# Kernel tuning notes

Measured on AMD Instinct MI355X. Metric: run time of the kernel, lower is better.

The kernel has to match this reference:

```python
import jax, jax.numpy as jnp
import numpy as np

N_PATHOLOGY = 14      # NUM_PATHOLOGY_NODES (CheXpert/NIH pathology count)
NEG_SLOPE = 0.2       # PyG GATv2Conv default negative_slope


def gatv2_layer(x, src, dst, n_nodes, Wl, bl, Wr, br, att, bias, concat):
    """PyG GATv2Conv (share_weights=False, dropout inactive in eval).
    Wl/bl: source (lin_l) transform; Wr/br: target (lin_r) transform.
    att: [H, C] attention vector; bias: output bias.
    """
    H, C = att.shape
    xl = (x @ Wl + bl).reshape(-1, H, C)   # [N, H, C] source features
    xr = (x @ Wr + br).reshape(-1, H, C)   # [N, H, C] target features
    xj = xl[src]                            # [E, H, C] gathered source msgs
    xi = xr[dst]                            # [E, H, C] gathered targets
    s = jax.nn.leaky_relu(xi + xj, NEG_SLOPE)
    e = jnp.einsum('ehc,hc->eh', s, att)    # [E, H] raw attention logits
    # segment softmax over incoming edges of each destination node
    m = jax.ops.segment_max(e, dst, num_segments=n_nodes)      # [N, H]
    e = jnp.exp(e - m[dst])
    denom = jax.ops.segment_sum(e, dst, num_segments=n_nodes)  # [N, H]
    alpha = e / (denom[dst] + 1e-16)
    out = jax.ops.segment_sum(alpha[:, :, None] * xj, dst, num_segments=n_nodes)
    out = out.reshape(n_nodes, H * C) if concat else out.mean(axis=1)
    return out + bias


def setup_inputs() -> dict:
    key = jax.random.key(0)
    ks = jax.random.split(key, 16)
    N, E, D, H = 10000, 50000, 768, 4
    s = 0.02
    inp = {
        'x': jax.random.normal(ks[0], (N, D), jnp.float32),
        'edge_index': jax.random.randint(ks[1], (2, E), 0, N, jnp.int32),
        # layer 1: in=768 -> heads=4, out=768 (concat -> 3072)
        'Wl1': jax.random.normal(ks[2], (D, H * D), jnp.float32) * s,
        'bl1': jnp.zeros((H * D,), jnp.float32),
        'Wr1': jax.random.normal(ks[3], (D, H * D), jnp.float32) * s,
        'br1': jnp.zeros((H * D,), jnp.float32),
        'att1': jax.random.normal(ks[4], (H, D), jnp.float32) * s,
        'bias1': jnp.zeros((H * D,), jnp.float32),
        # layer 2: in=3072 -> heads=1, out=768 (mean/no-concat)
        'Wl2': jax.random.normal(ks[5], (H * D, D), jnp.float32) * s,
        'bl2': jnp.zeros((D,), jnp.float32),
        'Wr2': jax.random.normal(ks[6], (H * D, D), jnp.float32) * s,
        'br2': jnp.zeros((D,), jnp.float32),
        'att2': jax.random.normal(ks[7], (1, D), jnp.float32) * s,
        'bias2': jnp.zeros((D,), jnp.float32),
    }
    return inp


def reference(x, edge_index, Wl1, bl1, Wr1, br1, att1, bias1,
              Wl2, bl2, Wr2, br2, att2, bias2):
    n = x.shape[0]
    # PyG GATv2Conv adds self loops by default
    loops = jnp.arange(n, dtype=edge_index.dtype)
    src = jnp.concatenate([edge_index[0], loops])
    dst = jnp.concatenate([edge_index[1], loops])
    h = gatv2_layer(x, src, dst, n, Wl1, bl1, Wr1, br1, att1, bias1, True)
    h = jax.nn.relu(h)  # dropout is identity in eval mode
    out = gatv2_layer(h, src, dst, n, Wl2, bl2, Wr2, br2, att2, bias2, False)
    return out[:N_PATHOLOGY]
```

## Files before the change

### kernel.cpp

```cpp
#include <hip/hip_runtime.h>
#include <cstdint>
#include <cstddef>

#define N_PATH 14
#define NEG_SLOPE 0.2f
#define BINW 128

using u16 = unsigned short;
using u32 = unsigned int;
typedef __attribute__((ext_vector_type(4))) float f32x4;
typedef __attribute__((ext_vector_type(8))) short bf16x8;

__device__ __forceinline__ float lrelu(float v) { return v > 0.f ? v : NEG_SLOPE * v; }
__device__ __forceinline__ u16 f2bf(float f) {
    union { float f; u32 u; } c; c.f = f;
    return (u16)((c.u + 0x7FFFu + ((c.u >> 16) & 1u)) >> 16);
}
__device__ __forceinline__ float bf2f(u16 v) {
    union { u32 u; float f; } c; c.u = ((u32)v) << 16; return c.f;
}

__global__ void k_init(int* __restrict__ mapBC, int nMap,
                       u32* __restrict__ z, int nZ)
{
    int stride = gridDim.x * blockDim.x;
    int i0 = blockIdx.x * blockDim.x + threadIdx.x;
    for (int i = i0; i < nMap; i += stride) mapBC[i] = -1;
    for (int i = i0; i < nZ; i += stride) z[i] = 0;
}

__global__ void k_build2(const int* __restrict__ esrc, const int* __restrict__ edst,
                         int E, int Nn,
                         int* __restrict__ mapB, int* __restrict__ listB,
                         int* __restrict__ cnt,
                         int* __restrict__ deg2, int* __restrict__ e2bin,
                         int capB)
{
    int e = blockIdx.x * blockDim.x + threadIdx.x;
    int ET = E + Nn;
    if (e >= ET) return;
    int s, d;
    if (e < E) { s = esrc[e]; d = edst[e]; } else { s = e - E; d = s; }
    if (d >= N_PATH) return;
    int slot = atomicAdd(&deg2[d], 1);
    if (slot < BINW) e2bin[d * BINW + slot] = s;
    int old = atomicCAS(&mapB[s], -1, -2);
    if (old == -1) {
        int idx = atomicAdd(&cnt[0], 1);
        if (idx < capB) listB[idx] = s;
        mapB[s] = idx;
    }
}

__global__ void k_build1(const int* __restrict__ esrc, const int* __restrict__ edst,
                         int E, int Nn,
                         const int* __restrict__ mapB,
                         int* __restrict__ mapC, int* __restrict__ listC,
                         int* __restrict__ cnt,
                         int* __restrict__ deg1, int* __restrict__ e1bin,
                         int capB, int capC)
{
    int e = blockIdx.x * blockDim.x + threadIdx.x;
    int ET = E + Nn;
    if (e >= ET) return;
    int s, d;
    if (e < E) { s = esrc[e]; d = edst[e]; } else { s = e - E; d = s; }
    int b = mapB[d];
    if (b < 0 || b >= capB) return;
    int slot = atomicAdd(&deg1[b], 1);
    if (slot < BINW) e1bin[b * BINW + slot] = s;
    int old = atomicCAS(&mapC[s], -1, -2);
    if (old == -1) {
        int idx = atomicAdd(&cnt[1], 1);
        if (idx < capC) listC[idx] = s;
        mapC[s] = idx;
    }
}

__device__ __forceinline__
void gemm_tile(const void* __restrict__ A, int lda, int aF32,
               const int* __restrict__ gather,
               const float* __restrict__ W, int ldw, int nColOff,
               const float* __restrict__ bias,
               void* __restrict__ Cout, int ldc, int mode, bool addBias,
               const int* __restrict__ cnt, int cntIdx, int capM,
               int bx, int by, int k0, int kchunk,
               u16* __restrict__ As, u16* __restrict__ Bs)
{
    int M = cnt[cntIdx]; if (M > capM) M = capM;
    int m0 = by * 64;
    if (m0 >= M) return;
    int n0 = bx * 64;
    int t = threadIdx.x;
    int lane = t & 63, wave = t >> 6;
    int wr = wave >> 1, wc = wave & 1;
    int lrow = lane & 15, lhi = lane >> 4;

    int chunk = t & 7;
    int rowp[2], aRow[2], wIdx[2];
    #pragma unroll
    for (int p = 0; p < 2; ++p) {
        rowp[p] = p * 32 + (t >> 3);
        int ar = m0 + rowp[p]; if (ar >= M) ar = M - 1;
        aRow[p] = gather ? gather[ar] : ar;
        wIdx[p] = rowp[p] * 64 + ((chunk ^ (rowp[p] & 7)) << 3);
    }
    int bk = t >> 4;
    int bn = (t & 15) << 2;

    int aIdx[2][2], bIdx[2][2];
    #pragma unroll
    for (int mi = 0; mi < 2; ++mi)
        #pragma unroll
        for (int ks = 0; ks < 2; ++ks) {
            int ra = wr * 32 + mi * 16 + lrow;
            aIdx[mi][ks] = ra * 64 + ((((ks << 2) | lhi) ^ (ra & 7)) << 3);
            int rb = wc * 32 + mi * 16 + lrow;
            bIdx[mi][ks] = rb * 64 + ((((ks << 2) | lhi) ^ (rb & 7)) << 3);
        }

    f32x4 acc[2][2];
    #pragma unroll
    for (int i = 0; i < 2; ++i)
        #pragma unroll
        for (int j = 0; j < 2; ++j)
            acc[i][j] = (f32x4){0.f, 0.f, 0.f, 0.f};

    for (int kt = 0; kt < kchunk; kt += 64) {
        int kb = k0 + kt;
        #pragma unroll
        for (int p = 0; p < 2; ++p) {
            uint4 av;
            if (aF32) {
                const float* ap = (const float*)A + (size_t)aRow[p] * lda + kb + chunk * 8;
                float4 f0 = *reinterpret_cast<const float4*>(ap);
                float4 f1 = *reinterpret_cast<const float4*>(ap + 4);
                av.x = (u32)f2bf(f0.x) | ((u32)f2bf(f0.y) << 16);
                av.y = (u32)f2bf(f0.z) | ((u32)f2bf(f0.w) << 16);
                av.z = (u32)f2bf(f1.x) | ((u32)f2bf(f1.y) << 16);
                av.w = (u32)f2bf(f1.z) | ((u32)f2bf(f1.w) << 16);
            } else {
                av = *reinterpret_cast<const uint4*>((const u16*)A + (size_t)aRow[p] * lda + kb + chunk * 8);
            }
            *reinterpret_cast<uint4*>(&As[wIdx[p]]) = av;
        }
        #pragma unroll
        for (int p = 0; p < 4; ++p) {
            int kk = p * 16 + bk;
            const float* wp = W + (size_t)(kb + kk) * ldw + nColOff + n0 + bn;
            float4 wv = *reinterpret_cast<const float4*>(wp);
            float wa[4] = {wv.x, wv.y, wv.z, wv.w};
            #pragma unroll
            for (int j = 0; j < 4; ++j) {
                int n = bn + j;
                int pc = (kk & 7) | ((((kk >> 3) & 7) ^ (n & 7)) << 3);
                Bs[n * 64 + pc] = f2bf(wa[j]);
            }
        }
        __syncthreads();
        #pragma unroll
        for (int ks = 0; ks < 2; ++ks) {
            bf16x8 a0 = *reinterpret_cast<const bf16x8*>(&As[aIdx[0][ks]]);
            bf16x8 a1 = *reinterpret_cast<const bf16x8*>(&As[aIdx[1][ks]]);
            bf16x8 b0 = *reinterpret_cast<const bf16x8*>(&Bs[bIdx[0][ks]]);
            bf16x8 b1 = *reinterpret_cast<const bf16x8*>(&Bs[bIdx[1][ks]]);
            acc[0][0] = __builtin_amdgcn_mfma_f32_16x16x32_bf16(a0, b0, acc[0][0], 0, 0, 0);
            acc[0][1] = __builtin_amdgcn_mfma_f32_16x16x32_bf16(a0, b1, acc[0][1], 0, 0, 0);
            acc[1][0] = __builtin_amdgcn_mfma_f32_16x16x32_bf16(a1, b0, acc[1][0], 0, 0, 0);
            acc[1][1] = __builtin_amdgcn_mfma_f32_16x16x32_bf16(a1, b1, acc[1][1], 0, 0, 0);
        }
        __syncthreads();
    }

    #pragma unroll
    for (int mi = 0; mi < 2; ++mi)
        #pragma unroll
        for (int ni = 0; ni < 2; ++ni) {
            int gc = n0 + wc * 32 + ni * 16 + lrow;
            float bv = addBias ? bias[gc] : 0.f;
            #pragma unroll
            for (int j = 0; j < 4; ++j) {
                int gr = m0 + wr * 32 + mi * 16 + lhi * 4 + j;
                if (gr < M) {
                    float v = acc[mi][ni][j] + bv;
                    if (mode == 2) ((u16*)Cout)[(size_t)gr * ldc + gc] = f2bf(v);
                    else           atomicAdd(&((float*)Cout)[(size_t)gr * ldc + gc], v);
                }
            }
        }
}

__global__ __launch_bounds__(256)
void k_gemm1(const float* __restrict__ x,
             const int* __restrict__ listC, const int* __restrict__ listB,
             const float* __restrict__ Wl1, const float* __restrict__ Wr1,
             const float* __restrict__ bl1, const float* __restrict__ br1,
             u16* __restrict__ XL1, u16* __restrict__ XR1,
             const int* __restrict__ cnt, int capC, int capB)
{
    __shared__ __align__(16) u16 As[64 * 64];
    __shared__ __align__(16) u16 Bs[64 * 64];
    int partA = 48 * (capC / 64);
    int bid = blockIdx.x;
    if (bid < partA) {
        gemm_tile(x, 768, 1, listC, Wl1, 3072, 0, bl1, XL1, 3072, 2, true,
                  cnt, 1, capC, bid % 48, bid / 48, 0, 768, As, Bs);
    } else {
        bid -= partA;
        gemm_tile(x, 768, 1, listB, Wr1, 3072, 0, br1, XR1, 3072, 2, true,
                  cnt, 0, capB, bid % 48, bid / 48, 0, 768, As, Bs);
    }
}

__global__ __launch_bounds__(256)
void k_gemm2(const u16* __restrict__ H1bf,
             const float* __restrict__ Wl2, const float* __restrict__ Wr2,
             const float* __restrict__ bl2, const float* __restrict__ br2,
             float* __restrict__ XLR2,
             const int* __restrict__ cnt, int capB)
{
    __shared__ __align__(16) u16 As[64 * 64];
    __shared__ __align__(16) u16 Bs[64 * 64];
    int bx = blockIdx.x;
    bool hi = bx >= 12;
    const float* W    = hi ? Wr2 : Wl2;
    const float* bias = hi ? br2 - 768 : bl2;
    int nColOff = hi ? -768 : 0;
    gemm_tile(H1bf, 3072, 0, nullptr, W, 768, nColOff, bias, XLR2, 1536, 1,
              blockIdx.z == 0, cnt, 0, capB, bx, blockIdx.y,
              blockIdx.z * 384, 384, As, Bs);
}

__global__ __launch_bounds__(256)
void k_fused1(const u16* __restrict__ XL1, const u16* __restrict__ XR1,
              const float* __restrict__ att1, const float* __restrict__ bias1,
              const int* __restrict__ mapC,
              const int* __restrict__ deg1, const int* __restrict__ e1bin,
              u16* __restrict__ H1bf,
              const int* __restrict__ cnt, int capB, int capC)
{
    __shared__ int sIdx[BINW];
    int b = blockIdx.x;
    int nB = cnt[0]; if (nB > capB) nB = capB;
    if (b >= nB) return;
    int t = threadIdx.x;
    int n = deg1[b]; if (n > BINW) n = BINW;
    if (t < n) {
        int c = mapC[e1bin[b * BINW + t]];
        if (c < 0) c = 0; if (c >= capC) c = capC - 1;
        sIdx[t] = c;
    }
    __syncthreads();

    int base = t * 12;
    float xr[12], av[12];
    {
        const u16* p = XR1 + (size_t)b * 3072 + base;
        uint2 q0 = *reinterpret_cast<const uint2*>(p);
        uint2 q1 = *reinterpret_cast<const uint2*>(p + 4);
        uint2 q2 = *reinterpret_cast<const uint2*>(p + 8);
        u32 w[6] = {q0.x, q0.y, q1.x, q1.y, q2.x, q2.y};
        #pragma unroll
        for (int j = 0; j < 6; ++j) {
            xr[2*j]   = bf2f((u16)(w[j] & 0xFFFF));
            xr[2*j+1] = bf2f((u16)(w[j] >> 16));
        }
        float4 a0 = *reinterpret_cast<const float4*>(att1 + base);
        float4 a1 = *reinterpret_cast<const float4*>(att1 + base + 4);
        float4 a2 = *reinterpret_cast<const float4*>(att1 + base + 8);
        av[0]=a0.x; av[1]=a0.y; av[2]=a0.z; av[3]=a0.w;
        av[4]=a1.x; av[5]=a1.y; av[6]=a1.z; av[7]=a1.w;
        av[8]=a2.x; av[9]=a2.y; av[10]=a2.z; av[11]=a2.w;
    }

    float acc[12];
    #pragma unroll
    for (int j = 0; j < 12; ++j) acc[j] = 0.f;
    float sumex = 0.f;

    uint2 q0, q1, q2;
    if (n > 0) {
        const u16* p = XL1 + (size_t)sIdx[0] * 3072 + base;
        q0 = *reinterpret_cast<const uint2*>(p);
        q1 = *reinterpret_cast<const uint2*>(p + 4);
        q2 = *reinterpret_cast<const uint2*>(p + 8);
    }
    for (int i = 0; i < n; ++i) {
        uint2 r0 = q0, r1 = q1, r2 = q2;
        if (i + 1 < n) {
            const u16* p = XL1 + (size_t)sIdx[i + 1] * 3072 + base;
            q0 = *reinterpret_cast<const uint2*>(p);
            q1 = *reinterpret_cast<const uint2*>(p + 4);
            q2 = *reinterpret_cast<const uint2*>(p + 8);
        }
        float xl[12];
        u32 w[6] = {r0.x, r0.y, r1.x, r1.y, r2.x, r2.y};
        #pragma unroll
        for (int j = 0; j < 6; ++j) {
            xl[2*j]   = bf2f((u16)(w[j] & 0xFFFF));
            xl[2*j+1] = bf2f((u16)(w[j] >> 16));
        }
        float pa = 0.f;
        #pragma unroll
        for (int j = 0; j < 12; ++j)
            pa = fmaf(av[j], lrelu(xl[j] + xr[j]), pa);
        #pragma unroll
        for (int off = 32; off > 0; off >>= 1) pa += __shfl_xor(pa, off);
        float ex = expf(pa);
        sumex += ex;
        #pragma unroll
        for (int j = 0; j < 12; ++j) acc[j] = fmaf(ex, xl[j], acc[j]);
    }

    float inv = 1.f / (sumex + 1e-16f);
    u32 o[6];
    #pragma unroll
    for (int j = 0; j < 6; ++j) {
        float v0 = acc[2*j]   * inv + bias1[base + 2*j];
        float v1 = acc[2*j+1] * inv + bias1[base + 2*j+1];
        v0 = v0 > 0.f ? v0 : 0.f;
        v1 = v1 > 0.f ? v1 : 0.f;
        o[j] = (u32)f2bf(v0) | ((u32)f2bf(v1) << 16);
    }
    u16* q = H1bf + (size_t)b * 3072 + base;
    uint2 s0; s0.x = o[0]; s0.y = o[1];
    uint2 s1; s1.x = o[2]; s1.y = o[3];
    uint2 s2; s2.x = o[4]; s2.y = o[5];
    *reinterpret_cast<uint2*>(q)     = s0;
    *reinterpret_cast<uint2*>(q + 4) = s1;
    *reinterpret_cast<uint2*>(q + 8) = s2;
}

__global__ __launch_bounds__(256)
void k_fused2(const float* __restrict__ XLR2,
              const float* __restrict__ att2, const float* __restrict__ bias2,
              const int* __restrict__ mapB,
              const int* __restrict__ deg2, const int* __restrict__ e2bin,
              float* __restrict__ out, int capB)
{
    __shared__ int sIdx[BINW];
    __shared__ float sAcc[4][768];
    __shared__ float sSum[4];
    int a = blockIdx.x;
    int t = threadIdx.x;
    int wv = t >> 6, lane = t & 63;
    int n = deg2[a]; if (n > BINW) n = BINW;
    if (t < n) {
        int bs = mapB[e2bin[a * BINW + t]];
        if (bs < 0) bs = 0; if (bs >= capB) bs = capB - 1;
        sIdx[t] = bs;
    }
    __syncthreads();

    int base = lane * 12;
    int bd = mapB[a];
    if (bd < 0) bd = 0; if (bd >= capB) bd = capB - 1;

    float xr[12], av[12];
    {
        const float* p = XLR2 + (size_t)bd * 1536 + 768 + base;
        float4 r0 = *reinterpret_cast<const float4*>(p);
        float4 r1 = *reinterpret_cast<const float4*>(p + 4);
        float4 r2 = *reinterpret_cast<const float4*>(p + 8);
        xr[0]=r0.x; xr[1]=r0.y; xr[2]=r0.z; xr[3]=r0.w;
        xr[4]=r1.x; xr[5]=r1.y; xr[6]=r1.z; xr[7]=r1.w;
        xr[8]=r2.x; xr[9]=r2.y; xr[10]=r2.z; xr[11]=r2.w;
        float4 a0 = *reinterpret_cast<const float4*>(att2 + base);
        float4 a1 = *reinterpret_cast<const float4*>(att2 + base + 4);
        float4 a2 = *reinterpret_cast<const float4*>(att2 + base + 8);
        av[0]=a0.x; av[1]=a0.y; av[2]=a0.z; av[3]=a0.w;
        av[4]=a1.x; av[5]=a1.y; av[6]=a1.z; av[7]=a1.w;
        av[8]=a2.x; av[9]=a2.y; av[10]=a2.z; av[11]=a2.w;
    }

    float acc[12];
    #pragma unroll
    for (int j = 0; j < 12; ++j) acc[j] = 0.f;
    float sumex = 0.f;

    for (int i = wv; i < n; i += 4) {
        int bs = sIdx[i];
        float xl[12];
        const float* p = XLR2 + (size_t)bs * 1536 + base;
        float4 r0 = *reinterpret_cast<const float4*>(p);
        float4 r1 = *reinterpret_cast<const float4*>(p + 4);
        float4 r2 = *reinterpret_cast<const float4*>(p + 8);
        xl[0]=r0.x; xl[1]=r0.y; xl[2]=r0.z; xl[3]=r0.w;
        xl[4]=r1.x; xl[5]=r1.y; xl[6]=r1.z; xl[7]=r1.w;
        xl[8]=r2.x; xl[9]=r2.y; xl[10]=r2.z; xl[11]=r2.w;
        float pa = 0.f;
        #pragma unroll
        for (int j = 0; j < 12; ++j)
            pa = fmaf(av[j], lrelu(xl[j] + xr[j]), pa);
        #pragma unroll
        for (int off = 32; off > 0; off >>= 1) pa += __shfl_xor(pa, off);
        float ex = expf(pa);
        sumex += ex;
        #pragma unroll
        for (int j = 0; j < 12; ++j) acc[j] = fmaf(ex, xl[j], acc[j]);
    }

    if (lane == 0) sSum[wv] = sumex;
    #pragma unroll
    for (int j = 0; j < 12; ++j) sAcc[wv][base + j] = acc[j];
    __syncthreads();

    float tot = sSum[0] + sSum[1] + sSum[2] + sSum[3];
    float inv = 1.f / (tot + 1e-16f);
    for (int c = t; c < 768; c += 256) {
        float s = sAcc[0][c] + sAcc[1][c] + sAcc[2][c] + sAcc[3][c];
        out[(size_t)a * 768 + c] = s * inv + bias2[c];
    }
}

struct Lay {
    size_t mapB, mapC;
    size_t zbase, zbytes;
    size_t cnt, deg2, deg1, XLR2;
    size_t listB, listC, e1bin, e2bin;
    size_t XL1, XR1, H1bf;
    size_t total;
};

static Lay makeLayout(int Nn, int cB, int cC)
{
    Lay L{};
    size_t off = 0;
    auto take = [&](size_t bytes) { size_t o = (off + 255) & ~(size_t)255; off = o + bytes; return o; };
    L.mapB = take((size_t)2 * Nn * 4);
    L.mapC = L.mapB + (size_t)Nn * 4;
    size_t zo = 0;
    size_t cntO  = zo; zo += 64;
    size_t deg2O = zo; zo += 64 * 4;
    size_t deg1O = zo; zo += (size_t)cB * 4;
    zo = (zo + 255) & ~(size_t)255;
    size_t xlr2O = zo; zo += (size_t)cB * 1536 * 4;
    L.zbase = take(zo); L.zbytes = zo;
    L.cnt  = L.zbase + cntO;
    L.deg2 = L.zbase + deg2O;
    L.deg1 = L.zbase + deg1O;
    L.XLR2 = L.zbase + xlr2O;
    L.listB = take((size_t)cB * 4);
    L.listC = take((size_t)cC * 4);
    L.e1bin = take((size_t)cB * BINW * 4);
    L.e2bin = take((size_t)16 * BINW * 4);
    L.XL1  = take((size_t)cC * 3072 * 2);
    L.XR1  = take((size_t)cB * 3072 * 2);
    L.H1bf = take((size_t)cB * 3072 * 2);
    L.total = off;
    return L;
}

extern "C" void kernel_launch(void* const* d_in, const int* in_sizes, int n_in,
                              void* d_out, int out_size, void* d_ws, size_t ws_size,
                              hipStream_t stream)
{
    const float* x     = (const float*)d_in[0];
    const int*   ei    = (const int*)  d_in[1];
    const float* Wl1   = (const float*)d_in[2];
    const float* bl1   = (const float*)d_in[3];
    const float* Wr1   = (const float*)d_in[4];
    const float* br1   = (const float*)d_in[5];
    const float* att1  = (const float*)d_in[6];
    const float* bias1 = (const float*)d_in[7];
    const float* Wl2   = (const float*)d_in[8];
    const float* bl2   = (const float*)d_in[9];
    const float* Wr2   = (const float*)d_in[10];
    const float* br2   = (const float*)d_in[11];
    const float* att2  = (const float*)d_in[12];
    const float* bias2 = (const float*)d_in[13];
    float* out = (float*)d_out;

    int Nn = in_sizes[0] / 768;
    int E  = in_sizes[1] / 2;
    const int* esrc = ei;
    const int* edst = ei + E;
    int ET = E + Nn;

    static const int tiers[2][2] = { {256, 1024}, {128, 768} };
    int capB = tiers[1][0], capC = tiers[1][1];
    Lay L = makeLayout(Nn, capB, capC);
    for (int t = 0; t < 2; ++t) {
        Lay cand = makeLayout(Nn, tiers[t][0], tiers[t][1]);
        if (cand.total <= ws_size) { capB = tiers[t][0]; capC = tiers[t][1]; L = cand; break; }
    }

    char* ws = (char*)d_ws;
    int*   mapB  = (int*)  (ws + L.mapB);
    int*   mapC  = (int*)  (ws + L.mapC);
    int*   cnt   = (int*)  (ws + L.cnt);
    int*   deg2  = (int*)  (ws + L.deg2);
    int*   deg1  = (int*)  (ws + L.deg1);
    float* XLR2  = (float*)(ws + L.XLR2);
    int*   listB = (int*)  (ws + L.listB);
    int*   listC = (int*)  (ws + L.listC);
    int*   e1bin = (int*)  (ws + L.e1bin);
    int*   e2bin = (int*)  (ws + L.e2bin);
    u16*   XL1   = (u16*)  (ws + L.XL1);
    u16*   XR1   = (u16*)  (ws + L.XR1);
    u16*   H1bf  = (u16*)  (ws + L.H1bf);

    k_init<<<512, 256, 0, stream>>>((int*)(ws + L.mapB), 2 * Nn,
                                    (u32*)(ws + L.zbase), (int)(L.zbytes / 4));

    int bgrid = (ET + 255) / 256;
    k_build2<<<bgrid, 256, 0, stream>>>(esrc, edst, E, Nn, mapB, listB, cnt,
                                        deg2, e2bin, capB);
    k_build1<<<bgrid, 256, 0, stream>>>(esrc, edst, E, Nn, mapB, mapC, listC, cnt,
                                        deg1, e1bin, capB, capC);

    int g1 = 48 * (capC / 64) + 48 * (capB / 64);
    k_gemm1<<<g1, 256, 0, stream>>>(x, listC, listB, Wl1, Wr1, bl1, br1,
                                    XL1, XR1, cnt, capC, capB);

    k_fused1<<<capB, 256, 0, stream>>>(XL1, XR1, att1, bias1, mapC, deg1, e1bin,
                                       H1bf, cnt, capB, capC);

    k_gemm2<<<dim3(24, capB / 64, 8), 256, 0, stream>>>(H1bf, Wl2, Wr2, bl2, br2,
                                                        XLR2, cnt, capB);

    k_fused2<<<N_PATH, 256, 0, stream>>>(XLR2, att2, bias2, mapB, deg2, e2bin,
                                         out, capB);
}
```

Measured before the change: 80.60 us.

## Restructure GEMMs with resident weight tiles, pre-converted bf16 A, split-K partial buffers

Adds a gather kernel that converts the needed x rows to bf16 once and maps B nodes onto C rows, so gemm1 reads bf16 A directly. A new templated GEMM core loads a whole K-panel of the weights into LDS once, then loops over row tiles while reading A fragments straight from global memory with double buffering. gemm2 now uses a two-way split-K that writes into two separate partial buffers instead of eight-way atomics, and fused2 sums the partials and adds the biases. The trade-offs are large LDS use (48KB per block), fewer blocks, and more global A traffic without LDS staging.

Result: slower. 106.6 us (+32.2%).

```diff
diff --git a/kernel.cpp b/kernel.cpp
--- a/kernel.cpp
+++ b/kernel.cpp
@@ -77,158 +77,174 @@
     }
 }
 
+__global__ void k_gatherA(const float* __restrict__ x,
+                          const int* __restrict__ listC, const int* __restrict__ listB,
+                          const int* __restrict__ mapC, const int* __restrict__ cnt,
+                          u16* __restrict__ Abf, int* __restrict__ listBinC,
+                          int capB, int capC)
+{
+    int bid = blockIdx.x;
+    int t = threadIdx.x;
+    if (bid == capC) {
+        int nB = cnt[0]; if (nB > capB) nB = capB;
+        for (int i = t; i < capB; i += 192) {
+            int v = 0;
+            if (i < nB) {
+                v = mapC[listB[i]];
+                if (v < 0) v = 0;
+                if (v >= capC) v = capC - 1;
+            }
+            listBinC[i] = v;
+        }
+        return;
+    }
+    int nC = cnt[1]; if (nC > capC) nC = capC;
+    if (bid >= nC) return;
+    int g = listC[bid];
+    float4 v = *reinterpret_cast<const float4*>(x + (size_t)g * 768 + t * 4);
+    uint2 o;
+    o.x = (u32)f2bf(v.x) | ((u32)f2bf(v.y) << 16);
+    o.y = (u32)f2bf(v.z) | ((u32)f2bf(v.w) << 16);
+    *reinterpret_cast<uint2*>(Abf + (size_t)bid * 768 + t * 4) = o;
+}
+
+template<int MF, int NWN, int KD, int MODE>
 __device__ __forceinline__
-void gemm_tile(const void* __restrict__ A, int lda, int aF32,
+void gemm_core(const u16* __restrict__ A, int lda,
                const int* __restrict__ gather,
-               const float* __restrict__ W, int ldw, int nColOff,
+               const float* __restrict__ W, int ldw,
                const float* __restrict__ bias,
-               void* __restrict__ Cout, int ldc, int mode, bool addBias,
-               const int* __restrict__ cnt, int cntIdx, int capM,
-               int bx, int by, int k0, int kchunk,
-               u16* __restrict__ As, u16* __restrict__ Bs)
-{
-    int M = cnt[cntIdx]; if (M > capM) M = capM;
-    int m0 = by * 64;
-    if (m0 >= M) return;
-    int n0 = bx * 64;
+               void* __restrict__ Cout, int ldc,
+               int M, int n0, int rt0, int rtStep,
+               u16* __restrict__ Bs)
+{
+    constexpr int WM = MF * 16;
+    constexpr int BM = (4 / NWN) * WM;
+    constexpr int BN = NWN * 16;
+    constexpr int NSTEP = KD / 64;
+    constexpr int NQ = BN / 4;
+
+    if (rt0 * BM >= M) return;
+
     int t = threadIdx.x;
     int lane = t & 63, wave = t >> 6;
-    int wr = wave >> 1, wc = wave & 1;
+    int wr = wave / NWN, wc = wave % NWN;
     int lrow = lane & 15, lhi = lane >> 4;
 
-    int chunk = t & 7;
-    int rowp[2], aRow[2], wIdx[2];
-    #pragma unroll
-    for (int p = 0; p < 2; ++p) {
-        rowp[p] = p * 32 + (t >> 3);
-        int ar = m0 + rowp[p]; if (ar >= M) ar = M - 1;
-        aRow[p] = gather ? gather[ar] : ar;
-        wIdx[p] = rowp[p] * 64 + ((chunk ^ (rowp[p] & 7)) << 3);
-    }
-    int bk = t >> 4;
-    int bn = (t & 15) << 2;
-
-    int aIdx[2][2], bIdx[2][2];
-    #pragma unroll
-    for (int mi = 0; mi < 2; ++mi)
-        #pragma unroll
-        for (int ks = 0; ks < 2; ++ks) {
-            int ra = wr * 32 + mi * 16 + lrow;
-            aIdx[mi][ks] = ra * 64 + ((((ks << 2) | lhi) ^ (ra & 7)) << 3);
-            int rb = wc * 32 + mi * 16 + lrow;
-            bIdx[mi][ks] = rb * 64 + ((((ks << 2) | lhi) ^ (rb & 7)) << 3);
-        }
-
-    f32x4 acc[2][2];
-    #pragma unroll
-    for (int i = 0; i < 2; ++i)
-        #pragma unroll
-        for (int j = 0; j < 2; ++j)
-            acc[i][j] = (f32x4){0.f, 0.f, 0.f, 0.f};
-
-    for (int kt = 0; kt < kchunk; kt += 64) {
-        int kb = k0 + kt;
-        #pragma unroll
-        for (int p = 0; p < 2; ++p) {
-            uint4 av;
-            if (aF32) {
-                const float* ap = (const float*)A + (size_t)aRow[p] * lda + kb + chunk * 8;
-                float4 f0 = *reinterpret_cast<const float4*>(ap);
-                float4 f1 = *reinterpret_cast<const float4*>(ap + 4);
-                av.x = (u32)f2bf(f0.x) | ((u32)f2bf(f0.y) << 16);
-                av.y = (u32)f2bf(f0.z) | ((u32)f2bf(f0.w) << 16);
-                av.z = (u32)f2bf(f1.x) | ((u32)f2bf(f1.y) << 16);
-                av.w = (u32)f2bf(f1.z) | ((u32)f2bf(f1.w) << 16);
-            } else {
-                av = *reinterpret_cast<const uint4*>((const u16*)A + (size_t)aRow[p] * lda + kb + chunk * 8);
+    for (int idx = t; idx < KD * NQ; idx += 256) {
+        int k = idx / NQ;
+        int n = (idx % NQ) * 4;
+        float4 wv = *reinterpret_cast<const float4*>(W + (size_t)k * ldw + n0 + n);
+        int c = k >> 3, kl = k & 7;
+        float wa[4] = {wv.x, wv.y, wv.z, wv.w};
+        #pragma unroll
+        for (int j = 0; j < 4; ++j) {
+            int nn = n + j;
+            Bs[nn * KD + (((c ^ (nn & 7)) << 3) | kl)] = f2bf(wa[j]);
+        }
+    }
+    __syncthreads();
+
+    int bcol = wc * 16 + lrow;
+    int bbase = bcol * KD;
+    int bx7 = bcol & 7;
+
+    for (int m0 = rt0 * BM; m0 < M; m0 += rtStep * BM) {
+        int arow[MF];
+        #pragma unroll
+        for (int mi = 0; mi < MF; ++mi) {
+            int r = m0 + wr * WM + mi * 16 + lrow;
+            if (r >= M) r = M - 1;
+            arow[mi] = gather ? gather[r] : r;
+        }
+        f32x4 acc[MF];
+        #pragma unroll
+        for (int mi = 0; mi < MF; ++mi) acc[mi] = (f32x4){0.f, 0.f, 0.f, 0.f};
+
+        uint4 abuf[2][MF][2];
+        #pragma unroll
+        for (int mi = 0; mi < MF; ++mi)
+            #pragma unroll
+            for (int ks = 0; ks < 2; ++ks)
+                abuf[0][mi][ks] = *reinterpret_cast<const uint4*>(
+                    A + (size_t)arow[mi] * lda + ks * 32 + lhi * 8);
+
+        #pragma unroll
+        for (int step = 0; step < NSTEP; ++step) {
+            int cur = step & 1, nxt = cur ^ 1;
+            if (step + 1 < NSTEP) {
+                int kb = (step + 1) * 64;
+                #pragma unroll
+                for (int mi = 0; mi < MF; ++mi)
+                    #pragma unroll
+                    for (int ks = 0; ks < 2; ++ks)
+                        abuf[nxt][mi][ks] = *reinterpret_cast<const uint4*>(
+                            A + (size_t)arow[mi] * lda + kb + ks * 32 + lhi * 8);
             }
-            *reinterpret_cast<uint4*>(&As[wIdx[p]]) = av;
-        }
-        #pragma unroll
-        for (int p = 0; p < 4; ++p) {
-            int kk = p * 16 + bk;
-            const float* wp = W + (size_t)(kb + kk) * ldw + nColOff + n0 + bn;
-            float4 wv = *reinterpret_cast<const float4*>(wp);
-            float wa[4] = {wv.x, wv.y, wv.z, wv.w};
+            #pragma unroll
+            for (int ks = 0; ks < 2; ++ks) {
+                int c = step * 8 + ks * 4 + lhi;
+                bf16x8 b = *reinterpret_cast<const bf16x8*>(&Bs[bbase + ((c ^ bx7) << 3)]);
+                #pragma unroll
+                for (int mi = 0; mi < MF; ++mi)
+                    acc[mi] = __builtin_amdgcn_mfma_f32_16x16x32_bf16(
+                        *reinterpret_cast<bf16x8*>(&abuf[cur][mi][ks]), b, acc[mi], 0, 0, 0);
+            }
+        }
+
+        int gc = n0 + wc * 16 + lrow;
+        float bv = 0.f;
+        if (MODE == 2) bv = bias[gc];
+        #pragma unroll
+        for (int mi = 0; mi < MF; ++mi)
             #pragma unroll
             for (int j = 0; j < 4; ++j) {
-                int n = bn + j;
-                int pc = (kk & 7) | ((((kk >> 3) & 7) ^ (n & 7)) << 3);
-                Bs[n * 64 + pc] = f2bf(wa[j]);
-            }
-        }
-        __syncthreads();
-        #pragma unroll
-        for (int ks = 0; ks < 2; ++ks) {
-            bf16x8 a0 = *reinterpret_cast<const bf16x8*>(&As[aIdx[0][ks]]);
-            bf16x8 a1 = *reinterpret_cast<const bf16x8*>(&As[aIdx[1][ks]]);
-            bf16x8 b0 = *reinterpret_cast<const bf16x8*>(&Bs[bIdx[0][ks]]);
-            bf16x8 b1 = *reinterpret_cast<const bf16x8*>(&Bs[bIdx[1][ks]]);
-            acc[0][0] = __builtin_amdgcn_mfma_f32_16x16x32_bf16(a0, b0, acc[0][0], 0, 0, 0);
-            acc[0][1] = __builtin_amdgcn_mfma_f32_16x16x32_bf16(a0, b1, acc[0][1], 0, 0, 0);
-            acc[1][0] = __builtin_amdgcn_mfma_f32_16x16x32_bf16(a1, b0, acc[1][0], 0, 0, 0);
-            acc[1][1] = __builtin_amdgcn_mfma_f32_16x16x32_bf16(a1, b1, acc[1][1], 0, 0, 0);
-        }
-        __syncthreads();
-    }
-
-    #pragma unroll
-    for (int mi = 0; mi < 2; ++mi)
-        #pragma unroll
-        for (int ni = 0; ni < 2; ++ni) {
-            int gc = n0 + wc * 32 + ni * 16 + lrow;
-            float bv = addBias ? bias[gc] : 0.f;
-            #pragma unroll
-            for (int j = 0; j < 4; ++j) {
-                int gr = m0 + wr * 32 + mi * 16 + lhi * 4 + j;
+                int gr = m0 + wr * WM + mi * 16 + lhi * 4 + j;
                 if (gr < M) {
-                    float v = acc[mi][ni][j] + bv;
-                    if (mode == 2) ((u16*)Cout)[(size_t)gr * ldc + gc] = f2bf(v);
-                    else           atomicAdd(&((float*)Cout)[(size_t)gr * ldc + gc], v);
+                    float v = acc[mi][j] + bv;
+                    if (MODE == 2) ((u16*)Cout)[(size_t)gr * ldc + gc] = f2bf(v);
+                    else           ((float*)Cout)[(size_t)gr * ldc + gc] = v;
                 }
             }
-        }
-}
-
-__global__ __launch_bounds__(256)
-void k_gemm1(const float* __restrict__ x,
-             const int* __restrict__ listC, const int* __restrict__ listB,
+    }
+}
+
+__global__ __launch_bounds__(256, 3)
+void k_gemm1(const u16* __restrict__ Abf, const int* __restrict__ listBinC,
              const float* __restrict__ Wl1, const float* __restrict__ Wr1,
              const float* __restrict__ bl1, const float* __restrict__ br1,
              u16* __restrict__ XL1, u16* __restrict__ XR1,
              const int* __restrict__ cnt, int capC, int capB)
 {
-    __shared__ __align__(16) u16 As[64 * 64];
-    __shared__ __align__(16) u16 Bs[64 * 64];
-    int partA = 48 * (capC / 64);
+    __shared__ __align__(16) u16 Bs[32 * 768];
     int bid = blockIdx.x;
-    if (bid < partA) {
-        gemm_tile(x, 768, 1, listC, Wl1, 3072, 0, bl1, XL1, 3072, 2, true,
-                  cnt, 1, capC, bid % 48, bid / 48, 0, 768, As, Bs);
+    if (bid < 192) {
+        int nC = cnt[1]; if (nC > capC) nC = capC;
+        gemm_core<4, 2, 768, 2>(Abf, 768, nullptr, Wl1, 3072, bl1,
+                                XL1, 3072, nC, (bid % 96) * 32, bid / 96, 2, Bs);
     } else {
-        bid -= partA;
-        gemm_tile(x, 768, 1, listB, Wr1, 3072, 0, br1, XR1, 3072, 2, true,
-                  cnt, 0, capB, bid % 48, bid / 48, 0, 768, As, Bs);
-    }
-}
-
-__global__ __launch_bounds__(256)
+        bid -= 192;
+        int nB = cnt[0]; if (nB > capB) nB = capB;
+        gemm_core<4, 2, 768, 2>(Abf, 768, listBinC, Wr1, 3072, br1,
+                                XR1, 3072, nB, bid * 32, 0, 1, Bs);
+    }
+}
+
+__global__ __launch_bounds__(256, 3)
 void k_gemm2(const u16* __restrict__ H1bf,
              const float* __restrict__ Wl2, const float* __restrict__ Wr2,
-             const float* __restrict__ bl2, const float* __restrict__ br2,
              float* __restrict__ XLR2,
              const int* __restrict__ cnt, int capB)
 {
-    __shared__ __align__(16) u16 As[64 * 64];
-    __shared__ __align__(16) u16 Bs[64 * 64];
-    int bx = blockIdx.x;
-    bool hi = bx >= 12;
-    const float* W    = hi ? Wr2 : Wl2;
-    const float* bias = hi ? br2 - 768 : bl2;
-    int nColOff = hi ? -768 : 0;
-    gemm_tile(H1bf, 3072, 0, nullptr, W, 768, nColOff, bias, XLR2, 1536, 1,
-              blockIdx.z == 0, cnt, 0, capB, bx, blockIdx.y,
-              blockIdx.z * 384, 384, As, Bs);
+    __shared__ __align__(16) u16 Bs[16 * 1536];
+    int nB = cnt[0]; if (nB > capB) nB = capB;
+    int z = blockIdx.z;
+    int n0 = blockIdx.x * 16;
+    bool hi = n0 >= 768;
+    const float* Wp = (hi ? Wr2 : Wl2) + (size_t)z * 1536 * 768 - (hi ? 768 : 0);
+    float* Cp = XLR2 + (size_t)z * capB * 1536;
+    gemm_core<2, 1, 1536, 0>(H1bf + (size_t)z * 1536, 3072, nullptr, Wp, 768,
+                             nullptr, Cp, 1536, nB, n0, 0, 1, Bs);
 }
 
 __global__ __launch_bounds__(256)
@@ -334,6 +350,7 @@
 __global__ __launch_bounds__(256)
 void k_fused2(const float* __restrict__ XLR2,
               const float* __restrict__ att2, const float* __restrict__ bias2,
+              const float* __restrict__ bl2, const float* __restrict__ br2,
               const int* __restrict__ mapB,
               const int* __restrict__ deg2, const int* __restrict__ e2bin,
               float* __restrict__ out, int capB)
@@ -341,6 +358,7 @@
     __shared__ int sIdx[BINW];
     __shared__ float sAcc[4][768];
     __shared__ float sSum[4];
+    const int PART = capB * 1536;
     int a = blockIdx.x;
     int t = threadIdx.x;
     int wv = t >> 6, lane = t & 63;
@@ -356,21 +374,13 @@
     int bd = mapB[a];
     if (bd < 0) bd = 0; if (bd >= capB) bd = capB - 1;
 
-    float xr[12], av[12];
+    float xr[12], av[12], blv[12];
     {
         const float* p = XLR2 + (size_t)bd * 1536 + 768 + base;
-        float4 r0 = *reinterpret_cast<const float4*>(p);
-        float4 r1 = *reinterpret_cast<const float4*>(p + 4);
-        float4 r2 = *reinterpret_cast<const float4*>(p + 8);
-        xr[0]=r0.x; xr[1]=r0.y; xr[2]=r0.z; xr[3]=r0.w;
-        xr[4]=r1.x; xr[5]=r1.y; xr[6]=r1.z; xr[7]=r1.w;
-        xr[8]=r2.x; xr[9]=r2.y; xr[10]=r2.z; xr[11]=r2.w;
-        float4 a0 = *reinterpret_cast<const float4*>(att2 + base);
-        float4 a1 = *reinterpret_cast<const float4*>(att2 + base + 4);
-        float4 a2 = *reinterpret_cast<const float4*>(att2 + base + 8);
-        av[0]=a0.x; av[1]=a0.y; av[2]=a0.z; av[3]=a0.w;
-        av[4]=a1.x; av[5]=a1.y; av[6]=a1.z; av[7]=a1.w;
-        av[8]=a2.x; av[9]=a2.y; av[10]=a2.z; av[11]=a2.w;
+        #pragma unroll
+        for (int j = 0; j < 12; ++j) xr[j] = p[j] + p[PART + j] + br2[base + j];
+        #pragma unroll
+        for (int j = 0; j < 12; ++j) { av[j] = att2[base + j]; blv[j] = bl2[base + j]; }
     }
 
     float acc[12];
@@ -380,14 +390,10 @@
 
     for (int i = wv; i < n; i += 4) {
         int bs = sIdx[i];
+        const float* p = XLR2 + (size_t)bs * 1536 + base;
         float xl[12];
-        const float* p = XLR2 + (size_t)bs * 1536 + base;
-        float4 r0 = *reinterpret_cast<const float4*>(p);
-        float4 r1 = *reinterpret_cast<const float4*>(p + 4);
-        float4 r2 = *reinterpret_cast<const float4*>(p + 8);
-        xl[0]=r0.x; xl[1]=r0.y; xl[2]=r0.z; xl[3]=r0.w;
-        xl[4]=r1.x; xl[5]=r1.y; xl[6]=r1.z; xl[7]=r1.w;
-        xl[8]=r2.x; xl[9]=r2.y; xl[10]=r2.z; xl[11]=r2.w;
+        #pragma unroll
+        for (int j = 0; j < 12; ++j) xl[j] = p[j] + p[PART + j] + blv[j];
         float pa = 0.f;
         #pragma unroll
         for (int j = 0; j < 12; ++j)
@@ -416,9 +422,9 @@
 struct Lay {
     size_t mapB, mapC;
     size_t zbase, zbytes;
-    size_t cnt, deg2, deg1, XLR2;
-    size_t listB, listC, e1bin, e2bin;
-    size_t XL1, XR1, H1bf;
+    size_t cnt, deg2, deg1;
+    size_t listB, listC, listBinC, e1bin, e2bin;
+    size_t Abf, XL1, XR1, H1bf, XLR2;
     size_t total;
 };
 
@@ -433,20 +439,20 @@
     size_t cntO  = zo; zo += 64;
     size_t deg2O = zo; zo += 64 * 4;
     size_t deg1O = zo; zo += (size_t)cB * 4;
-    zo = (zo + 255) & ~(size_t)255;
-    size_t xlr2O = zo; zo += (size_t)cB * 1536 * 4;
     L.zbase = take(zo); L.zbytes = zo;
     L.cnt  = L.zbase + cntO;
     L.deg2 = L.zbase + deg2O;
     L.deg1 = L.zbase + deg1O;
-    L.XLR2 = L.zbase + xlr2O;
-    L.listB = take((size_t)cB * 4);
-    L.listC = take((size_t)cC * 4);
+    L.listB    = take((size_t)cB * 4);
+    L.listC    = take((size_t)cC * 4);
+    L.listBinC = take((size_t)cB * 4);
     L.e1bin = take((size_t)cB * BINW * 4);
     L.e2bin = take((size_t)16 * BINW * 4);
+    L.Abf  = take((size_t)cC * 768 * 2);
     L.XL1  = take((size_t)cC * 3072 * 2);
     L.XR1  = take((size_t)cB * 3072 * 2);
     L.H1bf = take((size_t)cB * 3072 * 2);
+    L.XLR2 = take((size_t)2 * cB * 1536 * 4);
     L.total = off;
     return L;
 }
@@ -486,21 +492,23 @@
     }
 
     char* ws = (char*)d_ws;
-    int*   mapB  = (int*)  (ws + L.mapB);
-    int*   mapC  = (int*)  (ws + L.mapC);
-    int*   cnt   = (int*)  (ws + L.cnt);
-    int*   deg2  = (int*)  (ws + L.deg2);
-    int*   deg1  = (int*)  (ws + L.deg1);
-    float* XLR2  = (float*)(ws + L.XLR2);
-    int*   listB = (int*)  (ws + L.listB);
-    int*   listC = (int*)  (ws + L.listC);
-    int*   e1bin = (int*)  (ws + L.e1bin);
-    int*   e2bin = (int*)  (ws + L.e2bin);
-    u16*   XL1   = (u16*)  (ws + L.XL1);
-    u16*   XR1   = (u16*)  (ws + L.XR1);
-    u16*   H1bf  = (u16*)  (ws + L.H1bf);
-
-    k_init<<<512, 256, 0, stream>>>((int*)(ws + L.mapB), 2 * Nn,
+    int*   mapB     = (int*)  (ws + L.mapB);
+    int*   mapC     = (int*)  (ws + L.mapC);
+    int*   cnt      = (int*)  (ws + L.cnt);
+    int*   deg2     = (int*)  (ws + L.deg2);
+    int*   deg1     = (int*)  (ws + L.deg1);
+    int*   listB    = (int*)  (ws + L.listB);
+    int*   listC    = (int*)  (ws + L.listC);
+    int*   listBinC = (int*)  (ws + L.listBinC);
+    int*   e1bin    = (int*)  (ws + L.e1bin);
+    int*   e2bin    = (int*)  (ws + L.e2bin);
+    u16*   Abf      = (u16*)  (ws + L.Abf);
+    u16*   XL1      = (u16*)  (ws + L.XL1);
+    u16*   XR1      = (u16*)  (ws + L.XR1);
+    u16*   H1bf     = (u16*)  (ws + L.H1bf);
+    float* XLR2     = (float*)(ws + L.XLR2);
+
+    k_init<<<256, 256, 0, stream>>>((int*)(ws + L.mapB), 2 * Nn,
                                     (u32*)(ws + L.zbase), (int)(L.zbytes / 4));
 
     int bgrid = (ET + 255) / 256;
@@ -509,16 +517,17 @@
     k_build1<<<bgrid, 256, 0, stream>>>(esrc, edst, E, Nn, mapB, mapC, listC, cnt,
                                         deg1, e1bin, capB, capC);
 
-    int g1 = 48 * (capC / 64) + 48 * (capB / 64);
-    k_gemm1<<<g1, 256, 0, stream>>>(x, listC, listB, Wl1, Wr1, bl1, br1,
-                                    XL1, XR1, cnt, capC, capB);
+    k_gatherA<<<capC + 1, 192, 0, stream>>>(x, listC, listB, mapC, cnt,
+                                            Abf, listBinC, capB, capC);
+
+    k_gemm1<<<288, 256, 0, stream>>>(Abf, listBinC, Wl1, Wr1, bl1, br1,
+                                     XL1, XR1, cnt, capC, capB);
 
     k_fused1<<<capB, 256, 0, stream>>>(XL1, XR1, att1, bias1, mapC, deg1, e1bin,
                                        H1bf, cnt, capB, capC);
 
-    k_gemm2<<<dim3(24, capB / 64, 8), 256, 0, stream>>>(H1bf, Wl2, Wr2, bl2, br2,
-                                                        XLR2, cnt, capB);
-
-    k_fused2<<<N_PATH, 256, 0, stream>>>(XLR2, att2, bias2, mapB, deg2, e2bin,
-                                         out, capB);
-}
+    k_gemm2<<<dim3(96, 1, 2), 256, 0, stream>>>(H1bf, Wl2, Wr2, XLR2, cnt, capB);
+
+    k_fused2<<<N_PATH, 256, 0, stream>>>(XLR2, att2, bias2, bl2, br2, mapB,
+                                         deg2, e2bin, out, capB);
+}
```
